# Kernel optimization log

Measured on AMD Instinct MI355X. Metric: run time of the kernel, lower is better.

## Reference

```python
import jax, jax.numpy as jnp
import numpy as np

N_NODES = 200   # nlim = 50*4
EMB = 5
N_APPTYPES = 3
FEAT_IN = 50 * 52 + N_NODES  # 2800
B = 16384
E = 800


def setup_inputs() -> dict:
    key = jax.random.key(0)
    ks = jax.random.split(key, 16)
    x = jax.random.normal(ks[0], (B, 50, 52), dtype=jnp.float32)
    apps = jax.random.randint(ks[1], (B, N_NODES), 0, N_APPTYPES)
    edge_src = jax.random.randint(ks[2], (E,), 0, N_NODES)
    edge_dst = jax.random.randint(ks[3], (E,), 0, N_NODES)
    def lin(k, fan_in, fan_out):
        bound = 1.0 / np.sqrt(fan_in)
        kw, kb = jax.random.split(k)
        W = jax.random.uniform(kw, (fan_in, fan_out), minval=-bound, maxval=bound, dtype=jnp.float32)
        b = jax.random.uniform(kb, (fan_out,), minval=-bound, maxval=bound, dtype=jnp.float32)
        return W, b
    emb_table = jax.random.normal(ks[4], (N_APPTYPES, EMB), dtype=jnp.float32)
    gc_w, gc_b = lin(ks[5], EMB, 1)
    W1, b1 = lin(ks[6], FEAT_IN, 128)
    W2, b2 = lin(ks[7], 128, 128)
    W3, b3 = lin(ks[8], 128, 64)
    W4, b4 = lin(ks[9], 64, 2)
    return {"x": x, "apps": apps, "edge_src": edge_src, "edge_dst": edge_dst,
            "emb_table": emb_table, "gc_w": gc_w, "gc_b": gc_b,
            "W1": W1, "b1": b1, "W2": W2, "b2": b2,
            "W3": W3, "b3": b3, "W4": W4, "b4": b4}


def _graph_conv(h, edge_src, edge_dst, gc_w, gc_b):
    # DGL GraphConv, norm='both': D_in^{-1/2} A D_out^{-1/2} (X W) + b
    ones = jnp.ones((edge_src.shape[0],), dtype=h.dtype)
    deg_out = jnp.clip(jax.ops.segment_sum(ones, edge_src, num_segments=N_NODES), 1.0)
    deg_in = jnp.clip(jax.ops.segment_sum(ones, edge_dst, num_segments=N_NODES), 1.0)
    norm_src = deg_out ** -0.5  # [N]
    norm_dst = deg_in ** -0.5
    hw = h @ gc_w                       # [B, N, 1] (weight applied first: 5 > 1)
    msg = (hw * norm_src[None, :, None])[:, edge_src, :]      # [B, E, 1]
    agg = jnp.zeros_like(hw).at[:, edge_dst, :].add(msg)      # scatter-add over dst
    return agg * norm_dst[None, :, None] + gc_b


def reference(x, apps, edge_src, edge_dst, emb_table, gc_w, gc_b,
              W1, b1, W2, b2, W3, b3, W4, b4):
    h = emb_table[apps]                 # [B, 200, 5]; apps already length nlim -> zero-pad is no-op
    g = _graph_conv(h, edge_src, edge_dst, gc_w, gc_b)        # [B, 200, 1]
    feat = jnp.concatenate([x.reshape(x.shape[0], -1), g.reshape(g.shape[0], -1)], axis=-1)  # [B, 2800]
    a = jax.nn.softplus(feat @ W1 + b1)
    a = jax.nn.softplus(a @ W2 + b2)
    a = a @ W3 + b3
    a = a - jnp.tanh(a)                 # Tanhshrink
    out = jax.nn.sigmoid(a @ W4 + b4)   # [B, 2]
    return out
```

## Files before the change

kernel.cpp:

```cpp
#include <hip/hip_runtime.h>

#define NNODES 200
#define FEATX  2600
#define FEAT   2800
#define NC     88
#define N1     128

typedef _Float16 f16;
typedef _Float16 f16x8 __attribute__((ext_vector_type(8)));
typedef float    f32x4 __attribute__((ext_vector_type(4)));

#define W1P_OFF   0u
#define W2P_OFF   720896u
#define W3P_OFF   753664u
#define WG_OFF    770048u
#define B1P_OFF   821248u
#define HW_OFF    821760u
#define CSRP_OFF  821792u
#define CSRD_OFF  822608u
#define CSRW_OFF  825808u

__global__ __launch_bounds__(256)
void prepA(const int* __restrict__ esrc, const int* __restrict__ edst,
           const float* __restrict__ emb, const float* __restrict__ gcw,
           const float* __restrict__ gcb, const float* __restrict__ W1,
           const float* __restrict__ b1, char* __restrict__ ws) {
  __shared__ float dgo[NNODES], dgi[NNODES];
  __shared__ int   ssrc[800], sdst[800];
  __shared__ int   cnt[NNODES], cur[NNODES];
  __shared__ int   ps[256];
  __shared__ float red[256];
  const int tid = threadIdx.x;

  if (tid < NNODES) { dgo[tid] = 0.f; dgi[tid] = 0.f; cnt[tid] = 0; cur[tid] = 0; }
  __syncthreads();
  for (int e = tid; e < 800; e += 256) {
    const int s = esrc[e], d = edst[e];
    ssrc[e] = s; sdst[e] = d;
    atomicAdd(&dgo[s], 1.f);
    atomicAdd(&dgi[d], 1.f);
    atomicAdd(&cnt[s], 1);
  }
  __syncthreads();
  if (tid < NNODES) {
    dgo[tid] = 1.f / sqrtf(fmaxf(dgo[tid], 1.f));
    dgi[tid] = 1.f / sqrtf(fmaxf(dgi[tid], 1.f));
  }
  if (tid < 3) {
    float s = 0.f;
    for (int q = 0; q < 5; ++q) s += emb[tid * 5 + q] * gcw[q];
    ((float*)(ws + HW_OFF))[tid] = s;
  }
  ps[tid] = (tid < NNODES) ? cnt[tid] : 0;
  __syncthreads();
  for (int off = 1; off < 256; off <<= 1) {
    const int v = (tid >= off) ? ps[tid - off] : 0;
    __syncthreads();
    ps[tid] += v;
    __syncthreads();
  }
  int* rp = (int*)(ws + CSRP_OFF);
  if (tid < NNODES) rp[tid] = ps[tid] - cnt[tid];
  if (tid == NNODES) rp[NNODES] = 800;
  __syncthreads();
  int*   cd = (int*)(ws + CSRD_OFF);
  float* cw = (float*)(ws + CSRW_OFF);
  for (int e = tid; e < 800; e += 256) {
    const int s = ssrc[e], d = sdst[e];
    const int pos = (ps[s] - cnt[s]) + atomicAdd(&cur[s], 1);
    cd[pos] = d;
    cw[pos] = dgo[s] * dgi[d];
  }
  {
    const int j = tid & 127, h = tid >> 7;
    float s = 0.f;
    for (int d = h; d < NNODES; d += 2)
      s += W1[(FEATX + d) * N1 + j];
    red[tid] = s;
    __syncthreads();
    if (h == 0)
      ((float*)(ws + B1P_OFF))[j] = b1[j] + gcb[0] * (red[j] + red[128 + j]);
  }
}

__global__ __launch_bounds__(128)
void prepWg(const float* __restrict__ W1, char* __restrict__ ws) {
  const int n = blockIdx.x;
  const int j = threadIdx.x;
  const int* rp   = (const int*)(ws + CSRP_OFF);
  const int* cd   = (const int*)(ws + CSRD_OFF);
  const float* cw = (const float*)(ws + CSRW_OFF);
  const int e0 = rp[n], e1 = rp[n + 1];
  float acc = 0.f;
  for (int e = e0; e < e1; ++e)
    acc += cw[e] * W1[(FEATX + cd[e]) * N1 + j];
  ((f16*)(ws + WG_OFF))[n * N1 + j] = (f16)acc;
}

__global__ __launch_bounds__(256)
void pack(const float* __restrict__ W1, const float* __restrict__ W2,
          const float* __restrict__ W3, char* __restrict__ ws) {
  __shared__ __align__(16) float T[32 * 128];
  const int bid = blockIdx.x, tid = threadIdx.x;
  const f16* wg = (const f16*)(ws + WG_OFF);
  if (bid < NC) {
    const int k0 = bid * 32;
#pragma unroll
    for (int i = 0; i < 4; ++i) {
      const int p = i * 1024 + tid * 4;
      const int r = p >> 7, c = p & 127;
      const int k = k0 + r;
      float4 v;
      if (k < FEATX) v = *(const float4*)(W1 + (size_t)k * N1 + c);
      else if (k < FEAT) {
        const f16* g = wg + (k - FEATX) * N1 + c;
        v.x = (float)g[0]; v.y = (float)g[1]; v.z = (float)g[2]; v.w = (float)g[3];
      } else { v.x = v.y = v.z = v.w = 0.f; }
      *(float4*)(&T[r * 128 + c]) = v;
    }
    __syncthreads();
    char* dst = ws + W1P_OFF + (size_t)bid * 8192;
    for (int s = tid; s < 512; s += 256) {
      const int f = s >> 6, lx = s & 63;
      const int colb = f * 16 + (lx & 15), kb = (lx >> 4) * 8;
      union { f16x8 v; f16 h[8]; } u;
#pragma unroll
      for (int j = 0; j < 8; ++j) u.h[j] = (f16)T[(kb + j) * 128 + colb];
      *(f16x8*)(dst + f * 1024 + lx * 16) = u.v;
    }
  } else if (bid < 92) {
    const int cc = bid - 88, k0 = cc * 32;
#pragma unroll
    for (int i = 0; i < 4; ++i) {
      const int p = i * 1024 + tid * 4;
      const int r = p >> 7, c = p & 127;
      *(float4*)(&T[r * 128 + c]) = *(const float4*)(W2 + (size_t)(k0 + r) * 128 + c);
    }
    __syncthreads();
    char* dst = ws + W2P_OFF + (size_t)cc * 8192;
    for (int s = tid; s < 512; s += 256) {
      const int f = s >> 6, lx = s & 63;
      const int colb = f * 16 + (lx & 15), kb = (lx >> 4) * 8;
      union { f16x8 v; f16 h[8]; } u;
#pragma unroll
      for (int j = 0; j < 8; ++j) u.h[j] = (f16)T[(kb + j) * 128 + colb];
      *(f16x8*)(dst + f * 1024 + lx * 16) = u.v;
    }
  } else {
    const int cc = bid - 92, k0 = cc * 32;
#pragma unroll
    for (int i = 0; i < 2; ++i) {
      const int p = i * 1024 + tid * 4;
      const int r = p >> 6, c = p & 63;
      *(float4*)(&T[r * 64 + c]) = *(const float4*)(W3 + (size_t)(k0 + r) * 64 + c);
    }
    __syncthreads();
    char* dst = ws + W3P_OFF + (size_t)cc * 4096;
    {
      const int s = tid;
      const int f = s >> 6, lx = s & 63;
      const int colb = f * 16 + (lx & 15), kb = (lx >> 4) * 8;
      union { f16x8 v; f16 h[8]; } u;
#pragma unroll
      for (int j = 0; j < 8; ++j) u.h[j] = (f16)T[(kb + j) * 64 + colb];
      *(f16x8*)(dst + f * 1024 + lx * 16) = u.v;
    }
  }
}

__global__ __launch_bounds__(64)
void fused_main(const float* __restrict__ x, const int* __restrict__ apps,
                const char* __restrict__ ws, const float* __restrict__ b2,
                const float* __restrict__ b3, const float* __restrict__ W4,
                const float* __restrict__ b4, float* __restrict__ out) {
  __shared__ __align__(16) char lds[8192];
  const int l   = threadIdx.x;
  const int blk = blockIdx.x;
  const int lm  = l & 15, lg = l >> 4;
  const int row0 = blk * 32;

  const float* hwv = (const float*)(ws + HW_OFF);
  const float hw0 = hwv[0], hw1 = hwv[1], hw2 = hwv[2];

  const float* xr0 = x + (size_t)(row0 + lm) * FEATX;
  const float* xr1 = x + (size_t)(row0 + 16 + lm) * FEATX;
  const int*   ir0 = apps + (size_t)(row0 + lm) * NNODES;
  const int*   ir1 = apps + (size_t)(row0 + 16 + lm) * NNODES;
  const char*  w1p = ws + W1P_OFF;

  const f32x4 zed = {0.f, 0.f, 0.f, 0.f};
  f32x4 acc[2][8];
#pragma unroll
  for (int rt = 0; rt < 2; ++rt)
#pragma unroll
    for (int f = 0; f < 8; ++f) acc[rt][f] = zed;

  f16x8 B0[8], B1[8];
  uint4 A0[4], A1[4];
  f16x8 af[2];

  auto LB = [&](int c, f16x8* B) {
    const char* p = w1p + (size_t)(c > NC - 1 ? NC - 1 : c) * 8192 + l * 16;
#pragma unroll
    for (int f = 0; f < 8; ++f) B[f] = *(const f16x8*)(p + f * 1024);
  };
  auto LA = [&](int c, uint4* A) {
    const int k0 = (c > NC - 1 ? NC - 1 : c) * 32 + lg * 8;
    const char *p0, *p1;
    if (k0 + 8 <= FEATX) { p0 = (const char*)(xr0 + k0); p1 = (const char*)(xr1 + k0); }
    else if (k0 < FEAT)  { p0 = (const char*)(ir0 + (k0 - FEATX)); p1 = (const char*)(ir1 + (k0 - FEATX)); }
    else                 { p0 = (const char*)xr0; p1 = (const char*)xr1; }
    A[0] = *(const uint4*)p0; A[1] = *(const uint4*)(p0 + 16);
    A[2] = *(const uint4*)p1; A[3] = *(const uint4*)(p1 + 16);
  };
  auto CV = [&](int c, const uint4* A, f16x8* a2) {
    const int k0 = c * 32 + lg * 8;
#pragma unroll
    for (int rt = 0; rt < 2; ++rt) {
      union { uint4 u[2]; unsigned ui[8]; float f[8]; } d;
      d.u[0] = A[rt * 2]; d.u[1] = A[rt * 2 + 1];
      union { f16x8 v; f16 h[8]; } r;
      if (k0 + 8 <= FEATX) {
#pragma unroll
        for (int j = 0; j < 8; ++j) r.h[j] = (f16)d.f[j];
      } else if (k0 < FEAT) {
#pragma unroll
        for (int j = 0; j < 8; ++j) {
          const unsigned a = d.ui[j];
          r.h[j] = (f16)(a == 0u ? hw0 : (a == 1u ? hw1 : hw2));
        }
      } else {
#pragma unroll
        for (int j = 0; j < 8; ++j) r.h[j] = (f16)0.f;
      }
      a2[rt] = r.v;
    }
  };
  auto MM = [&](const f16x8* a2, const f16x8* B) {
#pragma unroll
    for (int f = 0; f < 8; ++f) {
      acc[0][f] = __builtin_amdgcn_mfma_f32_16x16x32_f16(a2[0], B[f], acc[0][f], 0, 0, 0);
      acc[1][f] = __builtin_amdgcn_mfma_f32_16x16x32_f16(a2[1], B[f], acc[1][f], 0, 0, 0);
    }
  };

  LA(0, A0); LB(0, B0); LA(1, A1);
#pragma unroll 1
  for (int c = 0; c < NC; c += 2) {
    LB(c + 1, B1);
    CV(c, A0, af);
    LA(c + 2, A0);
    MM(af, B0);
    LB(c + 2, B0);
    CV(c + 1, A1, af);
    LA(c + 3, A1);
    MM(af, B1);
  }

  const float* b1p = (const float*)(ws + B1P_OFF);
#pragma unroll
  for (int f = 0; f < 8; ++f) {
    const int col = f * 16 + lm;
    const float bb = b1p[col];
#pragma unroll
    for (int rt = 0; rt < 2; ++rt)
#pragma unroll
      for (int r = 0; r < 4; ++r) {
        const int row = rt * 16 + lg * 4 + r;
        float v = acc[rt][f][r] + bb;
        v = fmaxf(v, 0.f) + log1pf(expf(-fabsf(v)));
        *(f16*)(lds + ((row * 256 + col * 2) ^ ((row & 7) << 4))) = (f16)v;
      }
  }

  f32x4 c2[2][8];
#pragma unroll
  for (int rt = 0; rt < 2; ++rt)
#pragma unroll
    for (int f = 0; f < 8; ++f) c2[rt][f] = zed;
  const char* w2p = ws + W2P_OFF;
#pragma unroll
  for (int ks = 0; ks < 4; ++ks) {
    f16x8 bb2[8];
#pragma unroll
    for (int f = 0; f < 8; ++f)
      bb2[f] = *(const f16x8*)(w2p + ks * 8192 + f * 1024 + l * 16);
    f16x8 a2[2];
#pragma unroll
    for (int rt = 0; rt < 2; ++rt) {
      const int row = rt * 16 + lm;
      a2[rt] = *(const f16x8*)(lds + ((row * 256 + ks * 64 + lg * 16) ^ ((row & 7) << 4)));
    }
#pragma unroll
    for (int f = 0; f < 8; ++f) {
      c2[0][f] = __builtin_amdgcn_mfma_f32_16x16x32_f16(a2[0], bb2[f], c2[0][f], 0, 0, 0);
      c2[1][f] = __builtin_amdgcn_mfma_f32_16x16x32_f16(a2[1], bb2[f], c2[1][f], 0, 0, 0);
    }
  }
#pragma unroll
  for (int f = 0; f < 8; ++f) {
    const int col = f * 16 + lm;
    const float bb = b2[col];
#pragma unroll
    for (int rt = 0; rt < 2; ++rt)
#pragma unroll
      for (int r = 0; r < 4; ++r) {
        const int row = rt * 16 + lg * 4 + r;
        float v = c2[rt][f][r] + bb;
        v = fmaxf(v, 0.f) + log1pf(expf(-fabsf(v)));
        *(f16*)(lds + ((row * 256 + col * 2) ^ ((row & 7) << 4))) = (f16)v;
      }
  }

  f32x4 c3[2][4];
#pragma unroll
  for (int rt = 0; rt < 2; ++rt)
#pragma unroll
    for (int f = 0; f < 4; ++f) c3[rt][f] = zed;
  const char* w3p = ws + W3P_OFF;
#pragma unroll
  for (int ks = 0; ks < 4; ++ks) {
    f16x8 bb3[4];
#pragma unroll
    for (int f = 0; f < 4; ++f)
      bb3[f] = *(const f16x8*)(w3p + ks * 4096 + f * 1024 + l * 16);
    f16x8 a3[2];
#pragma unroll
    for (int rt = 0; rt < 2; ++rt) {
      const int row = rt * 16 + lm;
      a3[rt] = *(const f16x8*)(lds + ((row * 256 + ks * 64 + lg * 16) ^ ((row & 7) << 4)));
    }
#pragma unroll
    for (int f = 0; f < 4; ++f) {
      c3[0][f] = __builtin_amdgcn_mfma_f32_16x16x32_f16(a3[0], bb3[f], c3[0][f], 0, 0, 0);
      c3[1][f] = __builtin_amdgcn_mfma_f32_16x16x32_f16(a3[1], bb3[f], c3[1][f], 0, 0, 0);
    }
  }
#pragma unroll
  for (int f = 0; f < 4; ++f) {
    const int col = f * 16 + lm;
    const float bb = b3[col];
#pragma unroll
    for (int rt = 0; rt < 2; ++rt)
#pragma unroll
      for (int r = 0; r < 4; ++r) {
        const int row = rt * 16 + lg * 4 + r;
        const float z = c3[rt][f][r] + bb;
        *(float*)(lds + ((row * 256 + col * 4) ^ ((row & 7) << 4))) = z - tanhf(z);
      }
  }

  {
    const int row = l >> 1, j = l & 1;
    float s = 0.f;
#pragma unroll
    for (int kk = 0; kk < 16; ++kk) {
      const f32x4 a = *(const f32x4*)(lds + ((row * 256 + kk * 16) ^ ((row & 7) << 4)));
      s += a[0] * W4[(kk * 4 + 0) * 2 + j] + a[1] * W4[(kk * 4 + 1) * 2 + j]
         + a[2] * W4[(kk * 4 + 2) * 2 + j] + a[3] * W4[(kk * 4 + 3) * 2 + j];
    }
    s += b4[j];
    out[(size_t)(row0 + row) * 2 + j] = 1.f / (1.f + expf(-s));
  }
}

extern "C" void kernel_launch(void* const* d_in, const int* in_sizes, int n_in,
                              void* d_out, int out_size, void* d_ws, size_t ws_size,
                              hipStream_t stream) {
  const float* x    = (const float*)d_in[0];
  const int*   apps = (const int*)d_in[1];
  const int*   esrc = (const int*)d_in[2];
  const int*   edst = (const int*)d_in[3];
  const float* emb  = (const float*)d_in[4];
  const float* gcw  = (const float*)d_in[5];
  const float* gcb  = (const float*)d_in[6];
  const float* W1   = (const float*)d_in[7];
  const float* b1   = (const float*)d_in[8];
  const float* W2   = (const float*)d_in[9];
  const float* b2   = (const float*)d_in[10];
  const float* W3   = (const float*)d_in[11];
  const float* b3   = (const float*)d_in[12];
  const float* W4   = (const float*)d_in[13];
  const float* b4   = (const float*)d_in[14];
  char* ws = (char*)d_ws;
  float* out = (float*)d_out;

  hipLaunchKernelGGL(prepA, dim3(1), dim3(256), 0, stream,
                     esrc, edst, emb, gcw, gcb, W1, b1, ws);
  hipLaunchKernelGGL(prepWg, dim3(200), dim3(128), 0, stream, W1, ws);
  hipLaunchKernelGGL(pack, dim3(96), dim3(256), 0, stream, W1, W2, W3, ws);
  hipLaunchKernelGGL(fused_main, dim3(512), dim3(64), 0, stream,
                     x, apps, ws, b2, b3, W4, b4, out);
}
```

Before: 379.2 us.

## Stream W1 tiles into LDS via direct global-to-LDS loads and merge prep kernels

The main GEMM loop now brings the packed W1 B-tiles into a 4-slot LDS ring with global_load_lds instead of holding them in registers. Manual vmcnt waits and sched barriers keep several chunks in flight, which cuts register pressure and is meant to deepen the prefetch pipeline. Separately, the single-block CSR-building prep kernel and the per-node Wg kernel are replaced by one kernel in which each block scans the edge list itself, removing a launch and a serial prefix scan. The LDS footprint grows to 32 KB per 64-thread block, which may limit occupancy. The hand-counted vmcnt waits are fragile, and the B ring slots are reused with no barrier between waves.

Measured after the change: 515.9 us. +36.1%, slower.

```diff
diff --git a/kernel.cpp b/kernel.cpp
--- a/kernel.cpp
+++ b/kernel.cpp
@@ -16,85 +16,52 @@
 #define WG_OFF    770048u
 #define B1P_OFF   821248u
 #define HW_OFF    821760u
-#define CSRP_OFF  821792u
-#define CSRD_OFF  822608u
-#define CSRW_OFF  825808u
-
-__global__ __launch_bounds__(256)
-void prepA(const int* __restrict__ esrc, const int* __restrict__ edst,
+
+__device__ __forceinline__ void gl_lds16(const void* g, void* l) {
+  __builtin_amdgcn_global_load_lds(
+      (const __attribute__((address_space(1))) unsigned int*)g,
+      (__attribute__((address_space(3))) unsigned int*)l, 16, 0, 0);
+}
+
+__global__ __launch_bounds__(128)
+void prepG(const int* __restrict__ esrc, const int* __restrict__ edst,
            const float* __restrict__ emb, const float* __restrict__ gcw,
            const float* __restrict__ gcb, const float* __restrict__ W1,
            const float* __restrict__ b1, char* __restrict__ ws) {
-  __shared__ float dgo[NNODES], dgi[NNODES];
-  __shared__ int   ssrc[800], sdst[800];
-  __shared__ int   cnt[NNODES], cur[NNODES];
-  __shared__ int   ps[256];
-  __shared__ float red[256];
-  const int tid = threadIdx.x;
-
-  if (tid < NNODES) { dgo[tid] = 0.f; dgi[tid] = 0.f; cnt[tid] = 0; cur[tid] = 0; }
+  const int bid = blockIdx.x, tid = threadIdx.x;
+  if (bid == NNODES) {
+    float s = 0.f;
+    for (int d = 0; d < NNODES; ++d) s += W1[(FEATX + d) * N1 + tid];
+    ((float*)(ws + B1P_OFF))[tid] = b1[tid] + gcb[0] * s;
+    if (tid < 3) {
+      float h = 0.f;
+      for (int q = 0; q < 5; ++q) h += emb[tid * 5 + q] * gcw[q];
+      ((float*)(ws + HW_OFF))[tid] = h;
+    }
+    return;
+  }
+  __shared__ int din[NNODES];
+  __shared__ int mdst[128];
+  __shared__ int mcnt;
+  const int n = bid;
+  for (int i = tid; i < NNODES; i += 128) din[i] = 0;
+  if (tid == 0) mcnt = 0;
   __syncthreads();
-  for (int e = tid; e < 800; e += 256) {
-    const int s = esrc[e], d = edst[e];
-    ssrc[e] = s; sdst[e] = d;
-    atomicAdd(&dgo[s], 1.f);
-    atomicAdd(&dgi[d], 1.f);
-    atomicAdd(&cnt[s], 1);
+  for (int e = tid; e < 800; e += 128) {
+    const int d = edst[e];
+    atomicAdd(&din[d], 1);
+    if (esrc[e] == n) { const int p = atomicAdd(&mcnt, 1); if (p < 128) mdst[p] = d; }
   }
   __syncthreads();
-  if (tid < NNODES) {
-    dgo[tid] = 1.f / sqrtf(fmaxf(dgo[tid], 1.f));
-    dgi[tid] = 1.f / sqrtf(fmaxf(dgi[tid], 1.f));
-  }
-  if (tid < 3) {
-    float s = 0.f;
-    for (int q = 0; q < 5; ++q) s += emb[tid * 5 + q] * gcw[q];
-    ((float*)(ws + HW_OFF))[tid] = s;
-  }
-  ps[tid] = (tid < NNODES) ? cnt[tid] : 0;
-  __syncthreads();
-  for (int off = 1; off < 256; off <<= 1) {
-    const int v = (tid >= off) ? ps[tid - off] : 0;
-    __syncthreads();
-    ps[tid] += v;
-    __syncthreads();
-  }
-  int* rp = (int*)(ws + CSRP_OFF);
-  if (tid < NNODES) rp[tid] = ps[tid] - cnt[tid];
-  if (tid == NNODES) rp[NNODES] = 800;
-  __syncthreads();
-  int*   cd = (int*)(ws + CSRD_OFF);
-  float* cw = (float*)(ws + CSRW_OFF);
-  for (int e = tid; e < 800; e += 256) {
-    const int s = ssrc[e], d = sdst[e];
-    const int pos = (ps[s] - cnt[s]) + atomicAdd(&cur[s], 1);
-    cd[pos] = d;
-    cw[pos] = dgo[s] * dgi[d];
-  }
-  {
-    const int j = tid & 127, h = tid >> 7;
-    float s = 0.f;
-    for (int d = h; d < NNODES; d += 2)
-      s += W1[(FEATX + d) * N1 + j];
-    red[tid] = s;
-    __syncthreads();
-    if (h == 0)
-      ((float*)(ws + B1P_OFF))[j] = b1[j] + gcb[0] * (red[j] + red[128 + j]);
-  }
-}
-
-__global__ __launch_bounds__(128)
-void prepWg(const float* __restrict__ W1, char* __restrict__ ws) {
-  const int n = blockIdx.x;
-  const int j = threadIdx.x;
-  const int* rp   = (const int*)(ws + CSRP_OFF);
-  const int* cd   = (const int*)(ws + CSRD_OFF);
-  const float* cw = (const float*)(ws + CSRW_OFF);
-  const int e0 = rp[n], e1 = rp[n + 1];
+  const int deg = mcnt > 128 ? 128 : mcnt;
+  const float ns = 1.f / sqrtf(fmaxf((float)mcnt, 1.f));
   float acc = 0.f;
-  for (int e = e0; e < e1; ++e)
-    acc += cw[e] * W1[(FEATX + cd[e]) * N1 + j];
-  ((f16*)(ws + WG_OFF))[n * N1 + j] = (f16)acc;
+  for (int m = 0; m < deg; ++m) {
+    const int d = mdst[m];
+    const float w = ns / sqrtf(fmaxf((float)din[d], 1.f));
+    acc += w * W1[(FEATX + d) * N1 + tid];
+  }
+  ((f16*)(ws + WG_OFF))[n * N1 + tid] = (f16)acc;
 }
 
 __global__ __launch_bounds__(256)
@@ -173,7 +140,7 @@
                 const char* __restrict__ ws, const float* __restrict__ b2,
                 const float* __restrict__ b3, const float* __restrict__ W4,
                 const float* __restrict__ b4, float* __restrict__ out) {
-  __shared__ __align__(16) char lds[8192];
+  __shared__ __align__(16) char lds[32768];
   const int l   = threadIdx.x;
   const int blk = blockIdx.x;
   const int lm  = l & 15, lg = l >> 4;
@@ -195,16 +162,17 @@
 #pragma unroll
     for (int f = 0; f < 8; ++f) acc[rt][f] = zed;
 
-  f16x8 B0[8], B1[8];
   uint4 A0[4], A1[4];
   f16x8 af[2];
 
-  auto LB = [&](int c, f16x8* B) {
-    const char* p = w1p + (size_t)(c > NC - 1 ? NC - 1 : c) * 8192 + l * 16;
-#pragma unroll
-    for (int f = 0; f < 8; ++f) B[f] = *(const f16x8*)(p + f * 1024);
+  auto issueB = [&](int c) {
+    const int cc = c > NC - 1 ? NC - 1 : c;
+    const char* src = w1p + (size_t)cc * 8192 + l * 16;
+    char* dst = lds + (c & 3) * 8192;
+#pragma unroll
+    for (int f = 0; f < 8; ++f) gl_lds16(src + f * 1024, dst + f * 1024);
   };
-  auto LA = [&](int c, uint4* A) {
+  auto issueA = [&](int c, uint4* A) {
     const int k0 = (c > NC - 1 ? NC - 1 : c) * 32 + lg * 8;
     const char *p0, *p1;
     if (k0 + 8 <= FEATX) { p0 = (const char*)(xr0 + k0); p1 = (const char*)(xr1 + k0); }
@@ -236,26 +204,34 @@
       a2[rt] = r.v;
     }
   };
-  auto MM = [&](const f16x8* a2, const f16x8* B) {
+  auto MM = [&](const f16x8* a2, const char* bb) {
 #pragma unroll
     for (int f = 0; f < 8; ++f) {
-      acc[0][f] = __builtin_amdgcn_mfma_f32_16x16x32_f16(a2[0], B[f], acc[0][f], 0, 0, 0);
-      acc[1][f] = __builtin_amdgcn_mfma_f32_16x16x32_f16(a2[1], B[f], acc[1][f], 0, 0, 0);
+      const f16x8 bf = *(const f16x8*)(bb + f * 1024 + l * 16);
+      acc[0][f] = __builtin_amdgcn_mfma_f32_16x16x32_f16(a2[0], bf, acc[0][f], 0, 0, 0);
+      acc[1][f] = __builtin_amdgcn_mfma_f32_16x16x32_f16(a2[1], bf, acc[1][f], 0, 0, 0);
     }
   };
 
-  LA(0, A0); LB(0, B0); LA(1, A1);
+  issueB(0); issueA(0, A0); issueB(1); issueA(1, A1); issueB(2);
+  __builtin_amdgcn_sched_barrier(0);
+
 #pragma unroll 1
   for (int c = 0; c < NC; c += 2) {
-    LB(c + 1, B1);
+    asm volatile("s_waitcnt vmcnt(20)" ::: "memory");
     CV(c, A0, af);
-    LA(c + 2, A0);
-    MM(af, B0);
-    LB(c + 2, B0);
+    issueA(c + 2, A0);
+    issueB(c + 3);
+    __builtin_amdgcn_sched_barrier(0);
+    MM(af, lds + (c & 3) * 8192);
+    asm volatile("s_waitcnt vmcnt(20)" ::: "memory");
     CV(c + 1, A1, af);
-    LA(c + 3, A1);
-    MM(af, B1);
-  }
+    issueA(c + 3, A1);
+    issueB(c + 4);
+    __builtin_amdgcn_sched_barrier(0);
+    MM(af, lds + ((c + 1) & 3) * 8192);
+  }
+  asm volatile("s_waitcnt vmcnt(0)" ::: "memory");
 
   const float* b1p = (const float*)(ws + B1P_OFF);
 #pragma unroll
@@ -385,9 +361,8 @@
   char* ws = (char*)d_ws;
   float* out = (float*)d_out;
 
-  hipLaunchKernelGGL(prepA, dim3(1), dim3(256), 0, stream,
+  hipLaunchKernelGGL(prepG, dim3(NNODES + 1), dim3(128), 0, stream,
                      esrc, edst, emb, gcw, gcb, W1, b1, ws);
-  hipLaunchKernelGGL(prepWg, dim3(200), dim3(128), 0, stream, W1, ws);
   hipLaunchKernelGGL(pack, dim3(96), dim3(256), 0, stream, W1, W2, W3, ws);
   hipLaunchKernelGGL(fused_main, dim3(512), dim3(64), 0, stream,
                      x, apps, ws, b2, b3, W4, b4, out);
```
